# Performance work log

Hardware: AMD Instinct MI355X
Metric: run time of the kernel (lower is better)

Reference implementation:

```python
import jax, jax.numpy as jnp
from jax import lax
import numpy as np

B, C_IN, F, T = 8, 16, 1024, 512
D = 1024          # rnn_hidden_size == rnn_input_size
L = 4             # rnn_num_layers
N_TOKENS = 512
RES_REDUCE = 2


def setup_inputs() -> dict:
    key = jax.random.key(0)
    ks = jax.random.split(key, 8)
    fused_feats = jax.random.normal(ks[0], (B, C_IN, F, T), dtype=jnp.float32)
    s_audio_length = jax.random.randint(ks[1], (B,), 1, T + 1, dtype=jnp.int64)
    # 1x1 conv: C_IN -> 1 channel
    conv_w = jax.random.normal(ks[2], (C_IN,), dtype=jnp.float32) * (1.0 / np.sqrt(C_IN))
    conv_b = jnp.zeros((1,), dtype=jnp.float32)
    # SRU per-layer params (all layers have d_in == D): W [L, D, 3D], v [L, 2D], b [L, 2D]
    sru_W = jax.random.normal(ks[3], (L, D, 3 * D), dtype=jnp.float32) * (1.0 / np.sqrt(D))
    sru_v = jax.random.normal(ks[4], (L, 2 * D), dtype=jnp.float32) * 0.1
    sru_b = jnp.zeros((L, 2 * D), dtype=jnp.float32)
    fc_w = jax.random.normal(ks[5], (D, N_TOKENS), dtype=jnp.float32) * (1.0 / np.sqrt(D))
    fc_b = jnp.zeros((N_TOKENS,), dtype=jnp.float32)
    return dict(fused_feats=fused_feats, s_audio_length=s_audio_length,
                conv_w=conv_w, conv_b=conv_b,
                sru_W=sru_W, sru_v=sru_v, sru_b=sru_b,
                fc_w=fc_w, fc_b=fc_b)


def _sru_layer(x, W, v, b):
    # x: [T, B, D]; W: [D, 3D]; v, b: [2D]
    d = W.shape[1] // 3
    U = jnp.einsum('tbi,ik->tbk', x, W).reshape(x.shape[0], x.shape[1], 3, d)
    x_tilde, f_pre, r_pre = U[..., 0, :], U[..., 1, :], U[..., 2, :]
    vf, vr = v[:d], v[d:]
    bf, br = b[:d], b[d:]

    def step(c, inp):
        xt_t, fp_t = inp
        f = jax.nn.sigmoid(fp_t + vf * c + bf)
        c_new = f * c + (1.0 - f) * xt_t
        return c_new, c_new

    c0 = jnp.zeros((x.shape[1], d), dtype=x.dtype)
    _, cs = lax.scan(step, c0, (x_tilde, f_pre))            # cs: [T, B, D]
    r = jax.nn.sigmoid(r_pre + vr * cs + br)                # reset uses c_t
    return r * cs + (1.0 - r) * x                           # highway residual


def reference(fused_feats, s_audio_length, conv_w, conv_b, sru_W, sru_v, sru_b, fc_w, fc_b):
    # 1x1 conv over channel dim + ReLU: [B, C, F, T] -> [B, F, T]
    x = jax.nn.relu(jnp.einsum('bcft,c->bft', fused_feats, conv_w) + conv_b[0])
    x = x.transpose(2, 0, 1)                                # [T, B, F]
    for l in range(L):
        x = _sru_layer(x, sru_W[l], sru_v[l], sru_b[l])
    rnn_out = x.transpose(1, 0, 2)                          # [B, T, D]
    tokens_logits = jnp.einsum('btd,dk->btk', rnn_out, fc_w) + fc_b
    return tokens_logits, s_audio_length // RES_REDUCE
```

## Files before the change

kernel.cpp:

```cpp
#include <hip/hip_runtime.h>
#include <cstddef>
#include <cstdint>

static constexpr int B_  = 8;
static constexpr int CIN = 16;
static constexpr int F_  = 1024;
static constexpr int T_  = 512;
static constexpr int D_  = 1024;
static constexpr int L_  = 4;
static constexpr int NT  = 512;
static constexpr int M_  = T_ * B_;
static constexpr int K3  = 3 * D_;
static constexpr int NP  = 4 * D_;

typedef __attribute__((ext_vector_type(8))) short short8;
typedef __attribute__((ext_vector_type(4))) float floatx4;

__device__ __forceinline__ unsigned short f2bf(float f) {
    unsigned int u = __builtin_bit_cast(unsigned int, f);
    u += 0x7FFFu + ((u >> 16) & 1u);
    return (unsigned short)(u >> 16);
}
__device__ __forceinline__ float bf2f(unsigned short s) {
    unsigned int u = ((unsigned int)s) << 16;
    return __builtin_bit_cast(float, u);
}

#define GLD16(g, l)                                                              \
    __builtin_amdgcn_global_load_lds(                                            \
        (__attribute__((address_space(1))) unsigned int*)(g),                    \
        (__attribute__((address_space(3))) unsigned int*)(l), 16, 0, 0)

__global__ __launch_bounds__(256) void conv_relu_tr(
    const float* __restrict__ feats, const float* __restrict__ wv,
    const float* __restrict__ bv, unsigned short* __restrict__ x0) {
    __shared__ float tile[32][68];
    const int b  = blockIdx.z;
    const int f0 = blockIdx.y * 32;
    const int t0 = blockIdx.x * 64;
    const float bias = bv[0];

    const int t4 = threadIdx.x & 15;
    const int fi = threadIdx.x >> 4;
    #pragma unroll
    for (int fo = 0; fo < 32; fo += 16) {
        const int f = fo + fi;
        float4 acc = {bias, bias, bias, bias};
        const float* p = feats + (((size_t)b * CIN) * F_ + (f0 + f)) * T_ + t0 + t4 * 4;
        #pragma unroll
        for (int c = 0; c < CIN; ++c) {
            const float4 vv = *(const float4*)(p + (size_t)c * F_ * T_);
            const float w = wv[c];
            acc.x += w * vv.x; acc.y += w * vv.y;
            acc.z += w * vv.z; acc.w += w * vv.w;
        }
        acc.x = fmaxf(acc.x, 0.f); acc.y = fmaxf(acc.y, 0.f);
        acc.z = fmaxf(acc.z, 0.f); acc.w = fmaxf(acc.w, 0.f);
        *(float4*)&tile[f][t4 * 4] = acc;
    }
    __syncthreads();
    const int f4 = threadIdx.x & 7;
    const int tr = threadIdx.x >> 3;
    #pragma unroll
    for (int to = 0; to < 64; to += 32) {
        const int t = to + tr;
        unsigned short pk[4];
        #pragma unroll
        for (int q = 0; q < 4; ++q) pk[q] = f2bf(tile[f4 * 4 + q][t]);
        *(uint2*)&x0[(size_t)(t0 + t) * (B_ * D_) + (size_t)b * D_ + f0 + f4 * 4] =
            *(const uint2*)pk;
    }
}

__global__ __launch_bounds__(256) void prep_weights(
    const float* __restrict__ sru_W, const float* __restrict__ fc_w,
    unsigned short* __restrict__ Wt, unsigned short* __restrict__ WtF) {
    __shared__ float tile[32][33];
    const int z  = blockIdx.z;
    const int x  = threadIdx.x & 31;
    const int y8 = threadIdx.x >> 5;
    if (z < 16) {
        const int l = z >> 2, j = z & 3;
        const int d0 = blockIdx.x * 32;
        const int k0 = blockIdx.y * 32;
        unsigned short* Wo = Wt + (size_t)l * ((size_t)NP * D_);
        if (j < 3) {
            const float* W = sru_W + (size_t)l * D_ * K3;
            #pragma unroll
            for (int yo = 0; yo < 32; yo += 8)
                tile[yo + y8][x] = W[(size_t)(k0 + yo + y8) * K3 + j * D_ + d0 + x];
            __syncthreads();
            #pragma unroll
            for (int yo = 0; yo < 32; yo += 8) {
                const int dy = yo + y8;
                Wo[(size_t)((d0 + dy) * 4 + j) * D_ + k0 + x] = f2bf(tile[x][dy]);
            }
        } else {
            #pragma unroll
            for (int yo = 0; yo < 32; yo += 8) {
                const int dy = d0 + yo + y8;
                Wo[(size_t)(dy * 4 + 3) * D_ + k0 + x] =
                    (k0 + x == dy) ? (unsigned short)0x3F80u : (unsigned short)0u;
            }
        }
    } else {
        if (blockIdx.x >= NT / 32) return;
        const int n0 = blockIdx.x * 32;
        const int k0 = blockIdx.y * 32;
        #pragma unroll
        for (int yo = 0; yo < 32; yo += 8)
            tile[yo + y8][x] = fc_w[(size_t)(k0 + yo + y8) * NT + n0 + x];
        __syncthreads();
        #pragma unroll
        for (int yo = 0; yo < 32; yo += 8)
            WtF[(size_t)(n0 + yo + y8) * D_ + k0 + x] = f2bf(tile[x][yo + y8]);
    }
}

template <int MODE>
__global__ __launch_bounds__(256) void gemm_mfma(
    const unsigned short* __restrict__ A,
    const unsigned short* __restrict__ Bt,
    void* __restrict__ Cv, const float* __restrict__ bias,
    int N, int K) {
    __shared__ unsigned short As[128 * 32];
    __shared__ unsigned short Bs[128 * 32];

    const int tid  = threadIdx.x;
    const int lane = tid & 63;
    const int wid  = tid >> 6;
    const int m0 = blockIdx.y * 128;
    const int n0 = blockIdx.x * 128;
    const int wm = (wid >> 1) * 64;
    const int wn = (wid & 1) * 64;

    floatx4 acc[4][4];
    #pragma unroll
    for (int mi = 0; mi < 4; ++mi)
        #pragma unroll
        for (int ni = 0; ni < 4; ++ni)
            acc[mi][ni] = (floatx4){0.f, 0.f, 0.f, 0.f};

    const char* gA = (const char*)A;
    const char* gB = (const char*)Bt;
    const size_t rowstride = (size_t)K * 2;
    const size_t rA0 = (size_t)(m0 + (tid >> 2)) * rowstride + (tid & 3) * 16;
    const size_t rB0 = (size_t)(n0 + (tid >> 2)) * rowstride + (tid & 3) * 16;
    const size_t pstep = 64 * rowstride;
    char* sA = (char*)As;
    char* sB = (char*)Bs;
    const int ldsbase = wid * 1024;

    const int rsel = lane & 15;
    const int koff = (lane >> 4) * 16;

    for (int k0 = 0; k0 < K; k0 += 32) {
        const size_t kb = (size_t)k0 * 2;
        GLD16(gA + rA0 + kb,         sA + ldsbase);
        GLD16(gA + rA0 + kb + pstep, sA + ldsbase + 4096);
        GLD16(gB + rB0 + kb,         sB + ldsbase);
        GLD16(gB + rB0 + kb + pstep, sB + ldsbase + 4096);
        __syncthreads();

        short8 af[4], bfv[4];
        #pragma unroll
        for (int mi = 0; mi < 4; ++mi)
            af[mi] = *(const short8*)(sA + ((wm + mi * 16 + rsel) * 64 + koff));
        #pragma unroll
        for (int ni = 0; ni < 4; ++ni)
            bfv[ni] = *(const short8*)(sB + ((wn + ni * 16 + rsel) * 64 + koff));
        #pragma unroll
        for (int mi = 0; mi < 4; ++mi)
            #pragma unroll
            for (int ni = 0; ni < 4; ++ni)
                acc[mi][ni] = __builtin_amdgcn_mfma_f32_16x16x32_bf16(
                    af[mi], bfv[ni], acc[mi][ni], 0, 0, 0);
        __syncthreads();
    }

    const int cl = lane & 15;
    const int qr = lane >> 4;
    #pragma unroll
    for (int mi = 0; mi < 4; ++mi) {
        #pragma unroll
        for (int ni = 0; ni < 4; ++ni) {
            const int gn = n0 + wn + ni * 16 + cl;
            #pragma unroll
            for (int i = 0; i < 4; ++i) {
                const int gm = m0 + wm + mi * 16 + qr * 4 + i;
                if (MODE == 0) {
                    ((unsigned short*)Cv)[(size_t)gm * N + gn] = f2bf(acc[mi][ni][i]);
                } else {
                    const int t  = gm >> 3;
                    const int bb = gm & 7;
                    ((float*)Cv)[((size_t)bb * T_ + t) * NT + gn] =
                        acc[mi][ni][i] + bias[gn];
                }
            }
        }
    }
}

#define KT_BODY(CB, PB, KT2, DO_STAGE)                                        \
    {                                                                         \
        if (DO_STAGE) {                                                       \
            const size_t gk = (size_t)(KT2) * 64;                             \
            _Pragma("unroll") for (int s = 0; s < 2; ++s)                     \
                GLD16(Ab + (size_t)grow[s] * 2048 + gk + gcol[s],             \
                      (PB) + ((s * 8 + wid) << 10));                          \
            _Pragma("unroll") for (int s = 0; s < 2; ++s)                     \
                GLD16(Bb + (size_t)grow[s] * 2048 + gk + gcol[s],             \
                      (PB) + 16384 + ((s * 8 + wid) << 10));                  \
        }                                                                     \
        short8 af[8], bfv[4];                                                 \
        _Pragma("unroll") for (int mi = 0; mi < 8; ++mi)                      \
            af[mi] = *(const short8*)((CB) + aoff[mi]);                       \
        _Pragma("unroll") for (int ni = 0; ni < 4; ++ni)                      \
            bfv[ni] = *(const short8*)((CB) + boff[ni]);                      \
        __builtin_amdgcn_s_setprio(1);                                        \
        _Pragma("unroll") for (int mi = 0; mi < 8; ++mi)                      \
            _Pragma("unroll") for (int ni = 0; ni < 4; ++ni)                  \
                acc[mi][ni] = __builtin_amdgcn_mfma_f32_16x16x32_bf16(        \
                    af[mi], bfv[ni], acc[mi][ni], 0, 0, 0);                   \
        __builtin_amdgcn_s_setprio(0);                                        \
    }

__global__ __launch_bounds__(512, 2) void gemm256_gate(
    const unsigned short* __restrict__ A,
    const unsigned short* __restrict__ Bt,
    unsigned short* __restrict__ C) {
    __shared__ unsigned short lds[49152];
    char* const sb = (char*)lds;

    const int tid  = threadIdx.x;
    const int lane = tid & 63;
    const int wid  = tid >> 6;
    const int wm   = wid >> 2;
    const int wn   = wid & 3;
    const int m0   = blockIdx.y * 256;
    const int n0   = blockIdx.x * 256;

    const char* Ab = (const char*)A  + (size_t)m0 * 2048;
    const char* Bb = (const char*)Bt + (size_t)n0 * 2048;

    int grow[2], gcol[2];
    #pragma unroll
    for (int s = 0; s < 2; ++s) {
        const int q  = ((s * 8 + wid) << 10) + lane * 16;
        const int qs = q ^ (((q >> 7) & 3) << 4);
        grow[s] = qs >> 6;
        gcol[s] = qs & 63;
    }
    const int rl = lane & 15;
    const int kb = (lane >> 4) * 16;
    int aoff[8], boff[4];
    #pragma unroll
    for (int mi = 0; mi < 8; ++mi) {
        const int q = (wm * 128 + mi * 16 + rl) * 64 + kb;
        aoff[mi] = q ^ (((q >> 7) & 3) << 4);
    }
    #pragma unroll
    for (int ni = 0; ni < 4; ++ni) {
        const int q = (wn * 64 + ni * 16 + rl) * 64 + kb;
        boff[ni] = 16384 + (q ^ (((q >> 7) & 3) << 4));
    }

    floatx4 acc[8][4];
    #pragma unroll
    for (int mi = 0; mi < 8; ++mi)
        #pragma unroll
        for (int ni = 0; ni < 4; ++ni)
            acc[mi][ni] = (floatx4){0.f, 0.f, 0.f, 0.f};

    char* const b0 = sb;
    char* const b1 = sb + 32768;
    char* const b2 = sb + 65536;

    #pragma unroll
    for (int t = 0; t < 2; ++t) {
        char* pb = sb + t * 32768;
        const size_t gk = (size_t)t * 64;
        #pragma unroll
        for (int s = 0; s < 2; ++s)
            GLD16(Ab + (size_t)grow[s] * 2048 + gk + gcol[s],
                  pb + ((s * 8 + wid) << 10));
        #pragma unroll
        for (int s = 0; s < 2; ++s)
            GLD16(Bb + (size_t)grow[s] * 2048 + gk + gcol[s],
                  pb + 16384 + ((s * 8 + wid) << 10));
    }
    asm volatile("s_waitcnt vmcnt(4)" ::: "memory");
    __builtin_amdgcn_s_barrier();

    for (int kt = 0; kt < 30; kt += 3) {
        KT_BODY(b0, b2, kt + 2, true);
        asm volatile("s_waitcnt vmcnt(4)" ::: "memory");
        __builtin_amdgcn_s_barrier();
        KT_BODY(b1, b0, kt + 3, true);
        asm volatile("s_waitcnt vmcnt(4)" ::: "memory");
        __builtin_amdgcn_s_barrier();
        KT_BODY(b2, b1, kt + 4, true);
        asm volatile("s_waitcnt vmcnt(4)" ::: "memory");
        __builtin_amdgcn_s_barrier();
    }
    KT_BODY(b0, b2, 0, false);
    asm volatile("s_waitcnt vmcnt(0)" ::: "memory");
    __builtin_amdgcn_s_barrier();
    KT_BODY(b1, b0, 0, false);

    const int cl = lane & 15;
    const int qr = lane >> 4;
    #pragma unroll
    for (int mi = 0; mi < 8; ++mi) {
        #pragma unroll
        for (int ni = 0; ni < 4; ++ni) {
            const int gn = n0 + wn * 64 + ni * 16 + cl;
            #pragma unroll
            for (int i = 0; i < 4; ++i) {
                const int gm = m0 + wm * 128 + mi * 16 + qr * 4 + i;
                C[(size_t)gm * NP + gn] = f2bf(acc[mi][ni][i]);
            }
        }
    }
}

__global__ __launch_bounds__(64) void sru_scan(
    const unsigned short* __restrict__ U4,
    const float* __restrict__ v, const float* __restrict__ bvec,
    unsigned short* __restrict__ h) {
    const int idx = blockIdx.x * 64 + threadIdx.x;
    const int d  = idx & (D_ - 1);

    const float vfn = -v[d];
    const float vrn = -v[D_ + d];
    const float bf_ = bvec[d];
    const float br_ = bvec[D_ + d];

    const uint2* up = (const uint2*)U4 + idx;
    unsigned short* hp = h + idx;

    constexpr int UNR  = 8;
    constexpr int PIPE = 4;
    constexpr int NB   = T_ / UNR;
    constexpr size_t ST = (size_t)B_ * D_;

    uint2 ub[PIPE][UNR];
    #pragma unroll
    for (int p = 0; p < PIPE; ++p)
        #pragma unroll
        for (int j = 0; j < UNR; ++j)
            ub[p][j] = up[(size_t)(p * UNR + j) * ST];

    float c = 0.0f;
    for (int bt = 0; bt < NB; bt += PIPE) {
        #pragma unroll
        for (int p = 0; p < PIPE; ++p) {
            const int s = bt + p;
            #pragma unroll
            for (int j = 0; j < UNR; ++j) {
                const uint2 u = ub[p][j];
                const float xt  = bf2f((unsigned short)(u.x & 0xFFFFu));
                const float fpp = bf2f((unsigned short)(u.x >> 16));
                const float rpp = bf2f((unsigned short)(u.y & 0xFFFFu));
                const float xi  = bf2f((unsigned short)(u.y >> 16));
                const float e1 = __expf(fmaf(vfn, c, -(fpp + bf_)));
                const float f  = __builtin_amdgcn_rcpf(1.0f + e1);
                c = fmaf(f, c - xt, xt);
                const float e2 = __expf(fmaf(vrn, c, -(rpp + br_)));
                const float r  = __builtin_amdgcn_rcpf(1.0f + e2);
                hp[(size_t)(s * UNR + j) * ST] = f2bf(fmaf(r, c - xi, xi));
            }
            if (s + PIPE < NB) {
                #pragma unroll
                for (int j = 0; j < UNR; ++j)
                    ub[p][j] = up[(size_t)((s + PIPE) * UNR + j) * ST];
            }
        }
    }
}

__global__ void lens_k(const int* __restrict__ lens, float* __restrict__ out) {
    const int i = threadIdx.x;
    if (i < B_) out[i] = (float)(lens[i] >> 1);
}

extern "C" void kernel_launch(void* const* d_in, const int* in_sizes, int n_in,
                              void* d_out, int out_size, void* d_ws, size_t ws_size,
                              hipStream_t stream) {
    const float* feats  = (const float*)d_in[0];
    const int*   lens   = (const int*)d_in[1];
    const float* conv_w = (const float*)d_in[2];
    const float* conv_b = (const float*)d_in[3];
    const float* sru_W  = (const float*)d_in[4];
    const float* sru_v  = (const float*)d_in[5];
    const float* sru_b  = (const float*)d_in[6];
    const float* fc_w   = (const float*)d_in[7];
    const float* fc_b   = (const float*)d_in[8];
    float* out = (float*)d_out;

    unsigned short* x0 = (unsigned short*)d_ws;
    unsigned short* x1 = x0 + (size_t)M_ * D_;
    unsigned short* U4 = x1 + (size_t)M_ * D_;
    unsigned short* Wt = U4 + (size_t)M_ * NP;
    unsigned short* WtF = Wt + (size_t)L_ * NP * D_;

    conv_relu_tr<<<dim3(T_ / 64, F_ / 32, B_), 256, 0, stream>>>(
        feats, conv_w, conv_b, x0);

    prep_weights<<<dim3(32, 32, 17), 256, 0, stream>>>(sru_W, fc_w, Wt, WtF);

    unsigned short* cur = x0;
    unsigned short* nxt = x1;
    for (int l = 0; l < L_; ++l) {
        gemm256_gate<<<dim3(NP / 256, M_ / 256), 512, 0, stream>>>(
            cur, Wt + (size_t)l * NP * D_, U4);
        sru_scan<<<(B_ * D_) / 64, 64, 0, stream>>>(
            U4, sru_v + (size_t)l * 2 * D_, sru_b + (size_t)l * 2 * D_, nxt);
        unsigned short* tmp = cur; cur = nxt; nxt = tmp;
    }

    gemm_mfma<1><<<dim3(NT / 128, M_ / 128), 256, 0, stream>>>(
        cur, WtF, out, fc_b, NT, D_);

    lens_k<<<1, 64, 0, stream>>>(lens, out + (size_t)M_ * NT);
}
```

Measured before the change: 723.5 us.

## Split gate GEMM B staging around half-MFMA, fold lens into FC, use raw exp2

The gate GEMM inner body now issues the A-tile prefetch, runs MFMAs for the first two N sub-tiles, places a barrier, and only then issues the B-tile prefetch and runs the remaining MFMAs. The aim is to interleave global-to-LDS staging with compute and cut register pressure from the B fragments. The scan kernel folds log2(e) into its constants and calls v_exp_f32 directly, which removes the multiply that __expf adds on the serial recurrence path. The separate lens kernel is merged into the FC GEMM to save one launch. The extra barrier per K-step could add stalls, and staging B after the first compute half may race with reads of the current buffer if the buffer indexing is wrong.

```diff
diff --git a/kernel.cpp b/kernel.cpp
--- a/kernel.cpp
+++ b/kernel.cpp
@@ -117,11 +117,11 @@
     }
 }
 
-template <int MODE>
-__global__ __launch_bounds__(256) void gemm_mfma(
+__global__ __launch_bounds__(256) void gemm_fc(
     const unsigned short* __restrict__ A,
     const unsigned short* __restrict__ Bt,
-    void* __restrict__ Cv, const float* __restrict__ bias,
+    float* __restrict__ Cv, const float* __restrict__ bias,
+    const int* __restrict__ lens, float* __restrict__ lout,
     int N, int K) {
     __shared__ unsigned short As[128 * 32];
     __shared__ unsigned short Bs[128 * 32];
@@ -133,6 +133,9 @@
     const int n0 = blockIdx.x * 128;
     const int wm = (wid >> 1) * 64;
     const int wn = (wid & 1) * 64;
+
+    if (blockIdx.x == 0 && blockIdx.y == 0 && tid < B_)
+        lout[tid] = (float)(lens[tid] >> 1);
 
     floatx4 acc[4][4];
     #pragma unroll
@@ -188,14 +191,9 @@
             #pragma unroll
             for (int i = 0; i < 4; ++i) {
                 const int gm = m0 + wm + mi * 16 + qr * 4 + i;
-                if (MODE == 0) {
-                    ((unsigned short*)Cv)[(size_t)gm * N + gn] = f2bf(acc[mi][ni][i]);
-                } else {
-                    const int t  = gm >> 3;
-                    const int bb = gm & 7;
-                    ((float*)Cv)[((size_t)bb * T_ + t) * NT + gn] =
-                        acc[mi][ni][i] + bias[gn];
-                }
+                const int t  = gm >> 3;
+                const int bb = gm & 7;
+                Cv[((size_t)bb * T_ + t) * NT + gn] = acc[mi][ni][i] + bias[gn];
             }
         }
     }
@@ -203,25 +201,37 @@
 
 #define KT_BODY(CB, PB, KT2, DO_STAGE)                                        \
     {                                                                         \
-        if (DO_STAGE) {                                                       \
+        if (DO_STAGE) {      \
             const size_t gk = (size_t)(KT2) * 64;                             \
             _Pragma("unroll") for (int s = 0; s < 2; ++s)                     \
                 GLD16(Ab + (size_t)grow[s] * 2048 + gk + gcol[s],             \
                       (PB) + ((s * 8 + wid) << 10));                          \
+        }                                                                     \
+        short8 af[8], bf01[2], bf23[2];                                       \
+        _Pragma("unroll") for (int mi = 0; mi < 8; ++mi)                      \
+            af[mi] = *(const short8*)((CB) + aoff[mi]);                       \
+        _Pragma("unroll") for (int ni = 0; ni < 2; ++ni)                      \
+            bf01[ni] = *(const short8*)((CB) + boff[ni]);                     \
+        __builtin_amdgcn_s_setprio(1);                                        \
+        _Pragma("unroll") for (int mi = 0; mi < 8; ++mi)                      \
+            _Pragma("unroll") for (int ni = 0; ni < 2; ++ni)                  \
+                acc[mi][ni] = __builtin_amdgcn_mfma_f32_16x16x32_bf16(        \
+                    af[mi], bf01[ni], acc[mi][ni], 0, 0, 0);                  \
+        __builtin_amdgcn_s_setprio(0);                                        \
+        __builtin_amdgcn_s_barrier();                                         \
+        if (DO_STAGE) {      \
+            const size_t gk = (size_t)(KT2) * 64;                             \
             _Pragma("unroll") for (int s = 0; s < 2; ++s)                     \
                 GLD16(Bb + (size_t)grow[s] * 2048 + gk + gcol[s],             \
                       (PB) + 16384 + ((s * 8 + wid) << 10));                  \
         }                                                                     \
-        short8 af[8], bfv[4];                                                 \
-        _Pragma("unroll") for (int mi = 0; mi < 8; ++mi)                      \
-            af[mi] = *(const short8*)((CB) + aoff[mi]);                       \
-        _Pragma("unroll") for (int ni = 0; ni < 4; ++ni)                      \
-            bfv[ni] = *(const short8*)((CB) + boff[ni]);                      \
+        _Pragma("unroll") for (int ni = 0; ni < 2; ++ni)                      \
+            bf23[ni] = *(const short8*)((CB) + boff[2 + ni]);                 \
         __builtin_amdgcn_s_setprio(1);                                        \
         _Pragma("unroll") for (int mi = 0; mi < 8; ++mi)                      \
-            _Pragma("unroll") for (int ni = 0; ni < 4; ++ni)                  \
-                acc[mi][ni] = __builtin_amdgcn_mfma_f32_16x16x32_bf16(        \
-                    af[mi], bfv[ni], acc[mi][ni], 0, 0, 0);                   \
+            _Pragma("unroll") for (int ni = 0; ni < 2; ++ni)                  \
+                acc[mi][2 + ni] = __builtin_amdgcn_mfma_f32_16x16x32_bf16(    \
+                    af[mi], bf23[ni], acc[mi][2 + ni], 0, 0, 0);              \
         __builtin_amdgcn_s_setprio(0);                                        \
     }
 
@@ -331,10 +341,11 @@
     const int idx = blockIdx.x * 64 + threadIdx.x;
     const int d  = idx & (D_ - 1);
 
-    const float vfn = -v[d];
-    const float vrn = -v[D_ + d];
-    const float bf_ = bvec[d];
-    const float br_ = bvec[D_ + d];
+    constexpr float L2E = 1.44269504088896340736f;
+    const float vf2  = -v[d] * L2E;
+    const float vr2  = -v[D_ + d] * L2E;
+    const float mbfL = -bvec[d] * L2E;
+    const float mbrL = -bvec[D_ + d] * L2E;
 
     const uint2* up = (const uint2*)U4 + idx;
     unsigned short* hp = h + idx;
@@ -363,10 +374,14 @@
                 const float fpp = bf2f((unsigned short)(u.x >> 16));
                 const float rpp = bf2f((unsigned short)(u.y & 0xFFFFu));
                 const float xi  = bf2f((unsigned short)(u.y >> 16));
-                const float e1 = __expf(fmaf(vfn, c, -(fpp + bf_)));
+                const float pre1 = fmaf(fpp, -L2E, mbfL);
+                const float pre2 = fmaf(rpp, -L2E, mbrL);
+                float e1;
+                asm("v_exp_f32 %0, %1" : "=v"(e1) : "v"(fmaf(vf2, c, pre1)));
                 const float f  = __builtin_amdgcn_rcpf(1.0f + e1);
                 c = fmaf(f, c - xt, xt);
-                const float e2 = __expf(fmaf(vrn, c, -(rpp + br_)));
+                float e2;
+                asm("v_exp_f32 %0, %1" : "=v"(e2) : "v"(fmaf(vr2, c, pre2)));
                 const float r  = __builtin_amdgcn_rcpf(1.0f + e2);
                 hp[(size_t)(s * UNR + j) * ST] = f2bf(fmaf(r, c - xi, xi));
             }
@@ -377,11 +392,6 @@
             }
         }
     }
-}
-
-__global__ void lens_k(const int* __restrict__ lens, float* __restrict__ out) {
-    const int i = threadIdx.x;
-    if (i < B_) out[i] = (float)(lens[i] >> 1);
 }
 
 extern "C" void kernel_launch(void* const* d_in, const int* in_sizes, int n_in,
@@ -419,8 +429,6 @@
         unsigned short* tmp = cur; cur = nxt; nxt = tmp;
     }
 
-    gemm_mfma<1><<<dim3(NT / 128, M_ / 128), 256, 0, stream>>>(
-        cur, WtF, out, fc_b, NT, D_);
-
-    lens_k<<<1, 64, 0, stream>>>(lens, out + (size_t)M_ * NT);
-}
+    gemm_fc<<<dim3(NT / 128, M_ / 128), 256, 0, stream>>>(
+        cur, WtF, out, fc_b, lens, out + (size_t)M_ * NT, NT, D_);
+}
```

After: 709.7 us. Within noise of the previous version (-1.9%).
